# Optimization experiments

Measured on AMD Instinct MI355X. Metric: run time of the kernel, lower is better.

## Reference

```python
import jax, jax.numpy as jnp
import numpy as np

GS = 128      # quantization group size along K (in_features)
EPS = 1e-8

def setup_inputs() -> dict:
    key = jax.random.key(0)
    k1, k2, k3, k4 = jax.random.split(key, 4)
    B, S, K, N = 4, 2048, 4096, 4096
    x = jax.random.normal(k1, (B, S, K), dtype=jnp.float32)
    weight = jax.random.normal(k2, (N, K), dtype=jnp.float32) * 0.02   # torch Linear layout [out, in]
    bias = jax.random.normal(k3, (N,), dtype=jnp.float32) * 0.01
    # per-group (K//gs) x per-out-channel quant steps, strictly positive
    step_scales = jax.random.uniform(k4, (K // GS, N), dtype=jnp.float32, minval=0.01, maxval=0.05)
    return {"x": x, "weight": weight, "bias": bias, "step_scales": step_scales}

def reference(x, weight, bias, step_scales):
    # w: [K, N] (forward transposes the Linear weight)
    w = weight.T
    K, N = w.shape
    G = K // GS
    wg = w.reshape(G, GS, N)                       # group along K
    s = step_scales[:, None, :] + EPS              # [G, 1, N]
    # group-quantized dequant: round-to-step per (group, out-channel)
    q = jnp.round(wg / s)
    w_dq = (q * s).reshape(K, N)
    out = jnp.einsum('bsk,kn->bsn', x, w_dq)
    if bias is not None:
        out = out + bias
    return out
```

## Files before the change

### kernel.cpp

```cpp
#include <hip/hip_runtime.h>
#include <hip/hip_bf16.h>
#include <stdint.h>

typedef unsigned short u16;
typedef __bf16 bf16x8 __attribute__((ext_vector_type(8)));
typedef float f32x4 __attribute__((ext_vector_type(4)));
typedef unsigned short u16x8 __attribute__((ext_vector_type(8)));

#define QEPS 1e-8f

__device__ __forceinline__ u16 f32_to_bf16_rne(float f) {
    uint32_t u = __float_as_uint(f);
    u += 0x7fffu + ((u >> 16) & 1u);
    return (u16)(u >> 16);
}

__global__ void cvt_x_bf16(const float* __restrict__ x, u16* __restrict__ xb, int n8) {
    int idx = blockIdx.x * blockDim.x + threadIdx.x;
    if (idx >= n8) return;
    const float4* p = (const float4*)(x + (size_t)idx * 8);
    float4 a = p[0], b = p[1];
    u16x8 r;
    r[0] = f32_to_bf16_rne(a.x); r[1] = f32_to_bf16_rne(a.y);
    r[2] = f32_to_bf16_rne(a.z); r[3] = f32_to_bf16_rne(a.w);
    r[4] = f32_to_bf16_rne(b.x); r[5] = f32_to_bf16_rne(b.y);
    r[6] = f32_to_bf16_rne(b.z); r[7] = f32_to_bf16_rne(b.w);
    *(u16x8*)(xb + (size_t)idx * 8) = r;
}

__global__ void dequant_w_bf16(const float* __restrict__ w, const float* __restrict__ ss,
                               u16* __restrict__ wb, int N, int K) {
    int idx = blockIdx.x * blockDim.x + threadIdx.x;
    int pr = K >> 3;
    if (idx >= N * pr) return;
    int n = idx / pr;
    int k8 = (idx - n * pr) << 3;
    float s = ss[(size_t)(k8 >> 7) * N + n] + QEPS;
    const float4* p = (const float4*)(w + (size_t)n * K + k8);
    float4 a = p[0], b = p[1];
    float v[8] = {a.x, a.y, a.z, a.w, b.x, b.y, b.z, b.w};
    u16x8 r;
#pragma unroll
    for (int i = 0; i < 8; ++i) {
        float q = rintf(v[i] / s);
        r[i] = f32_to_bf16_rne(q * s);
    }
    *(u16x8*)(wb + (size_t)n * K + k8) = r;
}

#define BM 256
#define BN 256
#define SLOTB 32768
#define ABYT 16384
#define LDSB 131072

#define ASYNC16(g, l)                                                                      \
    __builtin_amdgcn_global_load_lds((const __attribute__((address_space(1))) void*)(g),   \
                                     (__attribute__((address_space(3))) void*)(l), 16, 0, 0)
#define VMCNT(n) asm volatile("s_waitcnt vmcnt(" #n ")" ::: "memory")
#define BAR()    __builtin_amdgcn_s_barrier()
#define MFMA(a, b, c) __builtin_amdgcn_mfma_f32_16x16x32_bf16((a), (b), (c), 0, 0, 0)

__global__ __launch_bounds__(512, 2) void gemm_bf16_bt_256(
        const u16* __restrict__ A,
        const u16* __restrict__ B,
        const float* __restrict__ bias,
        float* __restrict__ C,
        int M, int N, int K) {
    extern __shared__ char lds[];
    const int tid  = threadIdx.x;
    const int wave = tid >> 6;
    const int lane = tid & 63;

    const int nwg = gridDim.x;
    const int cpx = nwg >> 3;
    const int bid = blockIdx.x;
    const int swz = (bid & 7) * cpx + (bid >> 3);
    const int nbn = N / BN;
    const int bm  = swz / nbn;
    const int bn  = swz - bm * nbn;

    const int wr = wave >> 2;
    const int wc = wave & 3;

    const int srow  = tid >> 2;
    const int kbsrc = ((tid & 3) << 4) ^ (((tid >> 3) & 3) << 4);
    const char* gA0 = (const char*)A + ((size_t)(bm * BM + srow) * K) * 2 + kbsrc;
    const char* gA1 = (const char*)A + ((size_t)(bm * BM + 128 + srow) * K) * 2 + kbsrc;
    const char* gB0 = (const char*)B + ((size_t)(bn * BN + srow) * K) * 2 + kbsrc;
    const char* gB1 = (const char*)B + ((size_t)(bn * BN + 128 + srow) * K) * 2 + kbsrc;

    auto STAGE = [&](int t) {
        const size_t ko = (size_t)t << 6;
        char* d = lds + ((t & 3) * SLOTB) + (wave << 10);
        ASYNC16(gA0 + ko, d);
        ASYNC16(gA1 + ko, d + 8192);
        ASYNC16(gB0 + ko, d + ABYT);
        ASYNC16(gB1 + ko, d + ABYT + 8192);
    };

    const int kx = ((lane >> 4) ^ ((lane >> 1) & 3)) << 4;
    const char* pa = lds + (size_t)(wr * 128 + (lane & 15)) * 64 + kx;
    const char* pb = lds + ABYT + (size_t)(wc * 64 + (lane & 15)) * 64 + kx;

    f32x4 acc[8][4] = {};
    bf16x8 aX[8], bX[4], aY[8], bY[4];

#define RD_B(DST, i) DST[i] = *(const bf16x8*)(pb + bon + (i) * 1024)
#define RD_A(DST, i) DST[i] = *(const bf16x8*)(pa + bon + (i) * 1024)
#define MROW(CA, CB, m)                                                       \
    acc[m][0] = MFMA(CA[m], CB[0], acc[m][0]);                                \
    acc[m][1] = MFMA(CA[m], CB[1], acc[m][1]);                                \
    acc[m][2] = MFMA(CA[m], CB[2], acc[m][2]);                                \
    acc[m][3] = MFMA(CA[m], CB[3], acc[m][3]);

#define SLAB(CA, CB, NA, NB, t, DO_STAGE, DO_NEXT, VMSTMT)                    \
    {                                                                         \
        const int bon = (((t) + 1) & 3) * SLOTB;                              \
        if (DO_STAGE) STAGE((t) + 3);                                         \
        __builtin_amdgcn_s_setprio(1);                                        \
        MROW(CA, CB, 0)                                                       \
        if (DO_NEXT) { RD_B(NB, 0); RD_B(NB, 1); }                            \
        MROW(CA, CB, 1)                                                       \
        if (DO_NEXT) { RD_B(NB, 2); RD_B(NB, 3); }                            \
        MROW(CA, CB, 2)                                                       \
        if (DO_NEXT) { RD_A(NA, 0); RD_A(NA, 1); }                            \
        MROW(CA, CB, 3)                                                       \
        if (DO_NEXT) { RD_A(NA, 2); RD_A(NA, 3); }                            \
        MROW(CA, CB, 4)                                                       \
        if (DO_NEXT) { RD_A(NA, 4); RD_A(NA, 5); }                            \
        MROW(CA, CB, 5)                                                       \
        if (DO_NEXT) { RD_A(NA, 6); RD_A(NA, 7); }                            \
        MROW(CA, CB, 6)                                                       \
        MROW(CA, CB, 7)                                                       \
        __builtin_amdgcn_s_setprio(0);                                        \
        VMSTMT;                                                               \
        BAR();                                                                \
    }

    const int NT = K >> 5;

    STAGE(0); STAGE(1); STAGE(2);
    VMCNT(4);
    BAR();
    {
        const int bon = 0;
#pragma unroll
        for (int n = 0; n < 4; ++n) RD_B(bX, n);
#pragma unroll
        for (int m = 0; m < 8; ++m) RD_A(aX, m);
    }

    for (int t = 0; t < NT - 4; t += 2) {
        SLAB(aX, bX, aY, bY, t,     true, true, VMCNT(4))
        SLAB(aY, bY, aX, bX, t + 1, true, true, VMCNT(4))
    }
    SLAB(aX, bX, aY, bY, NT - 4, true,  true,  VMCNT(4))
    SLAB(aY, bY, aX, bX, NT - 3, false, true,  VMCNT(0))
    SLAB(aX, bX, aY, bY, NT - 2, false, true,  (void)0)
    SLAB(aY, bY, aX, bX, NT - 1, false, false, (void)0)

    const int r0 = bm * BM + wr * 128 + ((lane >> 4) << 2);
    const int c0 = bn * BN + wc * 64 + (lane & 15);
    float bv[4];
#pragma unroll
    for (int n = 0; n < 4; ++n) bv[n] = bias[c0 + n * 16];
#pragma unroll
    for (int m = 0; m < 8; ++m)
#pragma unroll
        for (int n = 0; n < 4; ++n)
#pragma unroll
            for (int i = 0; i < 4; ++i)
                C[(size_t)(r0 + m * 16 + i) * N + (c0 + n * 16)] = acc[m][n][i] + bv[n];
}

extern "C" void kernel_launch(void* const* d_in, const int* in_sizes, int n_in,
                              void* d_out, int out_size, void* d_ws, size_t ws_size,
                              hipStream_t stream) {
    const float* x    = (const float*)d_in[0];
    const float* w    = (const float*)d_in[1];
    const float* bias = (const float*)d_in[2];
    const float* ss   = (const float*)d_in[3];
    float* out        = (float*)d_out;

    const int N = in_sizes[2];
    const int K = in_sizes[1] / N;
    const int M = in_sizes[0] / K;

    u16* xb = (u16*)d_ws;
    u16* wb = xb + (size_t)M * K;

    int n8x = (M * K) >> 3;
    cvt_x_bf16<<<(n8x + 255) / 256, 256, 0, stream>>>(x, xb, n8x);

    int n8w = (N * K) >> 3;
    dequant_w_bf16<<<(n8w + 255) / 256, 256, 0, stream>>>(w, ss, wb, N, K);

    (void)hipFuncSetAttribute((const void*)gemm_bf16_bt_256,
                              hipFuncAttributeMaxDynamicSharedMemorySize, LDSB);
    dim3 grid((M / BM) * (N / BN));
    gemm_bf16_bt_256<<<grid, 512, LDSB, stream>>>(xb, wb, bias, out, M, N, K);
}
```

Measured before the change: 274.5 us.

## Load B operand directly from global into registers, bypassing LDS

The B (weight) tile is no longer staged through LDS. Each wave now loads its B fragments straight from global memory into registers one k-step ahead, and only A is staged in LDS, which halves the LDS footprint. The aim is to cut LDS traffic and capacity pressure. The cost is that the 4 waves sharing a column now each fetch the same B data from global memory, leaning on L2, and the global loads are strided by whole rows, so global-load latency is exposed more directly. The vmcnt waits are adjusted to account for the mixed load streams.

```diff
diff --git a/kernel.cpp b/kernel.cpp
--- a/kernel.cpp
+++ b/kernel.cpp
@@ -50,9 +50,8 @@
 
 #define BM 256
 #define BN 256
-#define SLOTB 32768
-#define ABYT 16384
-#define LDSB 131072
+#define SLOTB 16384
+#define LDSB 65536
 
 #define ASYNC16(g, l)                                                                      \
     __builtin_amdgcn_global_load_lds((const __attribute__((address_space(1))) void*)(g),   \
@@ -87,50 +86,50 @@
     const int kbsrc = ((tid & 3) << 4) ^ (((tid >> 3) & 3) << 4);
     const char* gA0 = (const char*)A + ((size_t)(bm * BM + srow) * K) * 2 + kbsrc;
     const char* gA1 = (const char*)A + ((size_t)(bm * BM + 128 + srow) * K) * 2 + kbsrc;
-    const char* gB0 = (const char*)B + ((size_t)(bn * BN + srow) * K) * 2 + kbsrc;
-    const char* gB1 = (const char*)B + ((size_t)(bn * BN + 128 + srow) * K) * 2 + kbsrc;
 
     auto STAGE = [&](int t) {
         const size_t ko = (size_t)t << 6;
         char* d = lds + ((t & 3) * SLOTB) + (wave << 10);
         ASYNC16(gA0 + ko, d);
         ASYNC16(gA1 + ko, d + 8192);
-        ASYNC16(gB0 + ko, d + ABYT);
-        ASYNC16(gB1 + ko, d + ABYT + 8192);
     };
 
     const int kx = ((lane >> 4) ^ ((lane >> 1) & 3)) << 4;
     const char* pa = lds + (size_t)(wr * 128 + (lane & 15)) * 64 + kx;
-    const char* pb = lds + ABYT + (size_t)(wc * 64 + (lane & 15)) * 64 + kx;
+
+    const u16* pbG = B + (size_t)(bn * BN + wc * 64 + (lane & 15)) * K + ((lane >> 4) << 3);
 
     f32x4 acc[8][4] = {};
     bf16x8 aX[8], bX[4], aY[8], bY[4];
 
-#define RD_B(DST, i) DST[i] = *(const bf16x8*)(pb + bon + (i) * 1024)
 #define RD_A(DST, i) DST[i] = *(const bf16x8*)(pa + bon + (i) * 1024)
+#define LD_B(DST, t)                                                          \
+    DST[0] = *(const bf16x8*)(pbG + (size_t)(t) * 32);                        \
+    DST[1] = *(const bf16x8*)(pbG + (size_t)16 * K + (size_t)(t) * 32);       \
+    DST[2] = *(const bf16x8*)(pbG + (size_t)32 * K + (size_t)(t) * 32);       \
+    DST[3] = *(const bf16x8*)(pbG + (size_t)48 * K + (size_t)(t) * 32);
 #define MROW(CA, CB, m)                                                       \
     acc[m][0] = MFMA(CA[m], CB[0], acc[m][0]);                                \
     acc[m][1] = MFMA(CA[m], CB[1], acc[m][1]);                                \
     acc[m][2] = MFMA(CA[m], CB[2], acc[m][2]);                                \
     acc[m][3] = MFMA(CA[m], CB[3], acc[m][3]);
 
-#define SLAB(CA, CB, NA, NB, t, DO_STAGE, DO_NEXT, VMSTMT)                    \
+#define SLAB(CA, CB, NA, NB, t, DO_STAGE, DO_BL, DO_WV, VMSTMT)               \
     {                                                                         \
         const int bon = (((t) + 1) & 3) * SLOTB;                              \
+        if (DO_BL) { LD_B(NB, (t) + 1) }                                      \
         if (DO_STAGE) STAGE((t) + 3);                                         \
         __builtin_amdgcn_s_setprio(1);                                        \
         MROW(CA, CB, 0)                                                       \
-        if (DO_NEXT) { RD_B(NB, 0); RD_B(NB, 1); }                            \
+        if (DO_WV) { RD_A(NA, 0); RD_A(NA, 1); }                              \
         MROW(CA, CB, 1)                                                       \
-        if (DO_NEXT) { RD_B(NB, 2); RD_B(NB, 3); }                            \
+        if (DO_WV) { RD_A(NA, 2); RD_A(NA, 3); }                              \
         MROW(CA, CB, 2)                                                       \
-        if (DO_NEXT) { RD_A(NA, 0); RD_A(NA, 1); }                            \
+        if (DO_WV) { RD_A(NA, 4); RD_A(NA, 5); }                              \
         MROW(CA, CB, 3)                                                       \
-        if (DO_NEXT) { RD_A(NA, 2); RD_A(NA, 3); }                            \
+        if (DO_WV) { RD_A(NA, 6); RD_A(NA, 7); }                              \
         MROW(CA, CB, 4)                                                       \
-        if (DO_NEXT) { RD_A(NA, 4); RD_A(NA, 5); }                            \
         MROW(CA, CB, 5)                                                       \
-        if (DO_NEXT) { RD_A(NA, 6); RD_A(NA, 7); }                            \
         MROW(CA, CB, 6)                                                       \
         MROW(CA, CB, 7)                                                       \
         __builtin_amdgcn_s_setprio(0);                                        \
@@ -140,25 +139,24 @@
 
     const int NT = K >> 5;
 
+    LD_B(bX, 0)
     STAGE(0); STAGE(1); STAGE(2);
-    VMCNT(4);
+    VMCNT(2);
     BAR();
     {
         const int bon = 0;
 #pragma unroll
-        for (int n = 0; n < 4; ++n) RD_B(bX, n);
-#pragma unroll
         for (int m = 0; m < 8; ++m) RD_A(aX, m);
     }
 
     for (int t = 0; t < NT - 4; t += 2) {
-        SLAB(aX, bX, aY, bY, t,     true, true, VMCNT(4))
-        SLAB(aY, bY, aX, bX, t + 1, true, true, VMCNT(4))
-    }
-    SLAB(aX, bX, aY, bY, NT - 4, true,  true,  VMCNT(4))
-    SLAB(aY, bY, aX, bX, NT - 3, false, true,  VMCNT(0))
-    SLAB(aX, bX, aY, bY, NT - 2, false, true,  (void)0)
-    SLAB(aY, bY, aX, bX, NT - 1, false, false, (void)0)
+        SLAB(aX, bX, aY, bY, t,     true, true, true, VMCNT(2))
+        SLAB(aY, bY, aX, bX, t + 1, true, true, true, VMCNT(2))
+    }
+    SLAB(aX, bX, aY, bY, NT - 4, true,  true,  true,  VMCNT(2))
+    SLAB(aY, bY, aX, bX, NT - 3, false, true,  true,  VMCNT(0))
+    SLAB(aX, bX, aY, bY, NT - 2, false, true,  true,  VMCNT(0))
+    SLAB(aY, bY, aX, bX, NT - 1, false, false, false, (void)0)
 
     const int r0 = bm * BM + wr * 128 + ((lane >> 4) << 2);
     const int c0 = bn * BN + wc * 64 + (lane & 15);
```

After: 415.3 us. 1.51x slower.
